# Kernel tuning notes

Measured on AMD Instinct MI355X. Metric: run time of the kernel, lower is better.

The kernel has to match this reference:

```python
import jax, jax.numpy as jnp
import numpy as np

B, E, N, F = 8, 2048, 2048, 128

def setup_inputs() -> dict:
    key = jax.random.key(0)
    k1, k2, k3, k4 = jax.random.split(key, 4)
    node_embeddings = jax.random.normal(k1, (B, N, F), dtype=jnp.float32)
    adj = jax.random.randint(k2, (B, E, N), -1, 3).astype(jnp.float32)
    W = jax.random.normal(k3, (F, F), dtype=jnp.float32) * (1.0 / np.sqrt(F))
    b = jax.random.normal(k4, (F,), dtype=jnp.float32) * 0.01
    return {"node_embeddings": node_embeddings, "adj": adj, "W": W, "b": b}

def reference(node_embeddings, adj, W, b):
    # adj_target: 1 where adj == -1, else 0
    adj_target = (adj == -1).astype(node_embeddings.dtype)          # [B, E, N]
    norm = jnp.sum(adj_target, axis=-1, keepdims=True)               # [B, E, 1]
    norm = jnp.where(norm == 0, 1.0, norm)
    # masked-mean aggregation of neighbor vertices into hyperedges
    message_vertex = jnp.matmul(adj_target, node_embeddings) / norm  # [B, E, F]
    # linear (torch Linear: x @ W.T + b) + relu
    hyperedge_embeddings = jax.nn.relu(jnp.matmul(message_vertex, W.T) + b)
    return hyperedge_embeddings
```

## Files before the change

### kernel.cpp

```cpp
#include <hip/hip_runtime.h>
#include <hip/hip_bf16.h>

#define B_ 8
#define E_ 2048
#define N_ 2048
#define F_ 128

#define BM 16
#define BK 64
#define MP 136

using bf16x8 = __bf16 __attribute__((ext_vector_type(8)));
using fx4    = float __attribute__((ext_vector_type(4)));

__global__ __launch_bounds__(256) void prep_node(const float* __restrict__ node,
                                                 __bf16* __restrict__ nodeT) {
    const int bid = blockIdx.x;
    const int b   = bid & 7;
    const int n0  = (bid >> 3) * 32;
    const int t   = threadIdx.x;
    const int f   = t & 127;
    const int nb  = n0 + (t >> 7) * 16;

    const float* src = node + ((size_t)b * N_ + nb) * F_ + f;
    __bf16 h[16];
#pragma unroll
    for (int i = 0; i < 16; ++i)
        h[i] = (__bf16)src[(size_t)i * F_];

    __bf16* dst = nodeT + ((size_t)b * F_ + f) * N_ + nb;
    *(uint4*)&dst[0] = *(const uint4*)&h[0];
    *(uint4*)&dst[8] = *(const uint4*)&h[8];
}

__global__ __launch_bounds__(256) void prep_w(const float* __restrict__ W,
                                              __bf16* __restrict__ Wb) {
    int idx = blockIdx.x * 256 + threadIdx.x;
    float4 v = *(const float4*)&W[idx * 4];
    __bf16 o[4] = {(__bf16)v.x, (__bf16)v.y, (__bf16)v.z, (__bf16)v.w};
    *(uint2*)&Wb[idx * 4] = *(const uint2*)o;
}

__global__ __launch_bounds__(256) void prep_adj(const float* __restrict__ adj,
                                                unsigned char* __restrict__ bitsT,
                                                float* __restrict__ rcount) {
    __shared__ __align__(16) unsigned char rowB[256];
    __shared__ float cw[4];
    const int row = blockIdx.x;
    const int t   = threadIdx.x;

    const float* src = adj + (size_t)row * N_ + t * 8;
    float4 v0 = *(const float4*)src;
    float4 v1 = *(const float4*)(src + 4);
    unsigned m = 0;
    m |= (v0.x == -1.f) ? 1u   : 0u;
    m |= (v0.y == -1.f) ? 2u   : 0u;
    m |= (v0.z == -1.f) ? 4u   : 0u;
    m |= (v0.w == -1.f) ? 8u   : 0u;
    m |= (v1.x == -1.f) ? 16u  : 0u;
    m |= (v1.y == -1.f) ? 32u  : 0u;
    m |= (v1.z == -1.f) ? 64u  : 0u;
    m |= (v1.w == -1.f) ? 128u : 0u;

    const int q  = t & 3;
    const int ks = (t >> 2) & 1;
    const int mm = t >> 3;
    rowB[q * 64 + mm * 2 + ks] = (unsigned char)m;

    float c = (float)__popc(m);
#pragma unroll
    for (int s = 1; s < 64; s <<= 1) c += __shfl_xor(c, s);
    if ((t & 63) == 0) cw[t >> 6] = c;
    __syncthreads();

    if (t < 64) {
        unsigned d = *(const unsigned*)&rowB[t * 4];
        *(unsigned*)&bitsT[(size_t)row * 256 + t * 4] = d;
    }
    if (t == 0) {
        float tot = cw[0] + cw[1] + cw[2] + cw[3];
        rcount[row] = 1.f / fmaxf(tot, 1.f);
    }
}

__global__ __launch_bounds__(256, 4) void v2h_main(const unsigned char* __restrict__ bitsT,
                                                   const __bf16* __restrict__ nodeT,
                                                   const __bf16* __restrict__ Wb,
                                                   const float* __restrict__ bias,
                                                   const float* __restrict__ rcount,
                                                   float* __restrict__ out) {
    __shared__ __align__(16) __bf16 Bs[2][128][64];
    __shared__ __align__(16) __bf16 Ms[BM * MP];

    const int t    = threadIdx.x;
    const int bid  = blockIdx.x;
    const int b    = bid & 7;
    const int e0   = (bid >> 3) * BM;
    const int w    = t >> 6;
    const int lane = t & 63;
    const int l15  = lane & 15;
    const int quad = lane >> 4;

    const __bf16* nTB = nodeT + (size_t)b * F_ * N_;

    auto issue_dma = [&](int k0, int buf) {
#pragma unroll
        for (int p = 0; p < 4; ++p) {
            int idx = t + 256 * p;
            int f   = idx >> 3;
            int sl  = idx & 7;
            int g   = sl ^ (f & 7);
            const __bf16* src = nTB + (size_t)f * N_ + k0 + g * 8;
            __bf16* dst = &Bs[buf][0][0] + (size_t)(w * 64 + 256 * p) * 8;
            __builtin_amdgcn_global_load_lds(
                (const __attribute__((address_space(1))) void*)src,
                (__attribute__((address_space(3))) void*)dst, 16, 0, 0);
        }
    };

    const unsigned char* rbP = bitsT + ((size_t)b * E_ + e0 + l15) * 256 + quad * 64;
    uint4 rb0 = *(const uint4*)(rbP +  0);
    uint4 rb1 = *(const uint4*)(rbP + 16);
    uint4 rb2 = *(const uint4*)(rbP + 32);
    uint4 rb3 = *(const uint4*)(rbP + 48);
    unsigned rw[16] = {rb0.x, rb0.y, rb0.z, rb0.w, rb1.x, rb1.y, rb1.z, rb1.w,
                       rb2.x, rb2.y, rb2.z, rb2.w, rb3.x, rb3.y, rb3.z, rb3.w};

    auto unpack = [](unsigned byte) -> bf16x8 {
        union { unsigned u[4]; bf16x8 v; } r;
        r.u[0] = ((byte &   1u) ? 0x3F80u : 0u) | ((byte &   2u) ? 0x3F800000u : 0u);
        r.u[1] = ((byte &   4u) ? 0x3F80u : 0u) | ((byte &   8u) ? 0x3F800000u : 0u);
        r.u[2] = ((byte &  16u) ? 0x3F80u : 0u) | ((byte &  32u) ? 0x3F800000u : 0u);
        r.u[3] = ((byte &  64u) ? 0x3F80u : 0u) | ((byte & 128u) ? 0x3F800000u : 0u);
        return r.v;
    };

    fx4 acc[2] = {};

    issue_dma(0, 0);

#pragma unroll
    for (int m = 0; m < 32; ++m) {
        const int buf = m & 1;
        __syncthreads();

        issue_dma(((m + 1) & 31) * BK, buf ^ 1);

        const unsigned word = rw[m >> 1];
        const int sh = 16 * (m & 1);
        bf16x8 af0 = unpack((word >> sh) & 255u);
        bf16x8 af1 = unpack((word >> (sh + 8)) & 255u);

#pragma unroll
        for (int ft = 0; ft < 2; ++ft) {
            int f  = w * 32 + ft * 16 + l15;
            int q0 = quad ^ (f & 7);
            int q1 = (4 + quad) ^ (f & 7);
            bf16x8 b0 = *(const bf16x8*)&Bs[buf][f][q0 * 8];
            acc[ft] = __builtin_amdgcn_mfma_f32_16x16x32_bf16(af0, b0, acc[ft], 0, 0, 0);
            bf16x8 b1 = *(const bf16x8*)&Bs[buf][f][q1 * 8];
            acc[ft] = __builtin_amdgcn_mfma_f32_16x16x32_bf16(af1, b1, acc[ft], 0, 0, 0);
        }
    }

    const int rbase = quad * 4;
    float rn[4];
#pragma unroll
    for (int r = 0; r < 4; ++r)
        rn[r] = rcount[(size_t)b * E_ + e0 + rbase + r];
#pragma unroll
    for (int ft = 0; ft < 2; ++ft) {
        int fcol = w * 32 + ft * 16 + l15;
#pragma unroll
        for (int r = 0; r < 4; ++r)
            Ms[(rbase + r) * MP + fcol] = (__bf16)(acc[ft][r] * rn[r]);
    }
    __syncthreads();

    fx4 acc2[2] = {};
#pragma unroll
    for (int ks = 0; ks < 4; ++ks) {
        bf16x8 afm = *(const bf16x8*)&Ms[l15 * MP + ks * 32 + quad * 8];
#pragma unroll
        for (int gt = 0; gt < 2; ++gt) {
            int g = w * 32 + gt * 16 + l15;
            bf16x8 wfr = *(const bf16x8*)&Wb[(size_t)g * F_ + ks * 32 + quad * 8];
            acc2[gt] = __builtin_amdgcn_mfma_f32_16x16x32_bf16(afm, wfr, acc2[gt], 0, 0, 0);
        }
    }

#pragma unroll
    for (int gt = 0; gt < 2; ++gt) {
        int g = w * 32 + gt * 16 + l15;
        float bb = bias[g];
#pragma unroll
        for (int r = 0; r < 4; ++r) {
            int e = e0 + rbase + r;
            float v = acc2[gt][r] + bb;
            out[((size_t)b * E_ + e) * F_ + g] = fmaxf(v, 0.f);
        }
    }
}

extern "C" void kernel_launch(void* const* d_in, const int* in_sizes, int n_in,
                              void* d_out, int out_size, void* d_ws, size_t ws_size,
                              hipStream_t stream) {
    const float* node = (const float*)d_in[0];
    const float* adj  = (const float*)d_in[1];
    const float* W    = (const float*)d_in[2];
    const float* bias = (const float*)d_in[3];
    float* out = (float*)d_out;

    char* ws = (char*)d_ws;
    __bf16*        nodeT = (__bf16*)ws;
    __bf16*        Wb    = (__bf16*)(ws + 8 * 1024 * 1024);
    unsigned char* bitsT = (unsigned char*)(ws + 8 * 1024 * 1024 + 65536);
    float*         rcnt  = (float*)(ws + 12 * 1024 * 1024 + 65536);

    prep_node<<<512, 256, 0, stream>>>(node, nodeT);
    prep_w<<<16, 256, 0, stream>>>(W, Wb);
    prep_adj<<<B_ * E_, 256, 0, stream>>>(adj, bitsT, rcnt);
    v2h_main<<<1024, 256, 0, stream>>>(bitsT, nodeT, Wb, bias, rcnt, out);
}
```

Measured before the change: 230.6 us.

## Merge prep kernels into one launch and double hyperedge rows per block

Combines the three preprocessing kernels (node transpose, weight cast, adjacency bitmask) into one kernel that branches on block index, which saves two launches. The main kernel now handles 32 hyperedge rows per block instead of 16, so each staged node tile in LDS feeds twice as many MFMAs and total node-tile traffic is halved. The cost is more registers per thread (launch bounds lowered to 2 waves per SIMD) and half as many blocks (512), which may reduce occupancy and latency hiding.

```diff
diff --git a/kernel.cpp b/kernel.cpp
--- a/kernel.cpp
+++ b/kernel.cpp
@@ -6,84 +6,81 @@
 #define N_ 2048
 #define F_ 128
 
-#define BM 16
+#define BM 32
 #define BK 64
 #define MP 136
 
 using bf16x8 = __bf16 __attribute__((ext_vector_type(8)));
 using fx4    = float __attribute__((ext_vector_type(4)));
 
-__global__ __launch_bounds__(256) void prep_node(const float* __restrict__ node,
-                                                 __bf16* __restrict__ nodeT) {
-    const int bid = blockIdx.x;
-    const int b   = bid & 7;
-    const int n0  = (bid >> 3) * 32;
-    const int t   = threadIdx.x;
-    const int f   = t & 127;
-    const int nb  = n0 + (t >> 7) * 16;
-
-    const float* src = node + ((size_t)b * N_ + nb) * F_ + f;
-    __bf16 h[16];
-#pragma unroll
-    for (int i = 0; i < 16; ++i)
-        h[i] = (__bf16)src[(size_t)i * F_];
-
-    __bf16* dst = nodeT + ((size_t)b * F_ + f) * N_ + nb;
-    *(uint4*)&dst[0] = *(const uint4*)&h[0];
-    *(uint4*)&dst[8] = *(const uint4*)&h[8];
-}
-
-__global__ __launch_bounds__(256) void prep_w(const float* __restrict__ W,
-                                              __bf16* __restrict__ Wb) {
-    int idx = blockIdx.x * 256 + threadIdx.x;
-    float4 v = *(const float4*)&W[idx * 4];
-    __bf16 o[4] = {(__bf16)v.x, (__bf16)v.y, (__bf16)v.z, (__bf16)v.w};
-    *(uint2*)&Wb[idx * 4] = *(const uint2*)o;
-}
-
-__global__ __launch_bounds__(256) void prep_adj(const float* __restrict__ adj,
+__global__ __launch_bounds__(256) void prep_all(const float* __restrict__ node,
+                                                const float* __restrict__ adj,
+                                                const float* __restrict__ W,
+                                                __bf16* __restrict__ nodeT,
+                                                __bf16* __restrict__ Wb,
                                                 unsigned char* __restrict__ bitsT,
                                                 float* __restrict__ rcount) {
     __shared__ __align__(16) unsigned char rowB[256];
     __shared__ float cw[4];
-    const int row = blockIdx.x;
+    const int bid = blockIdx.x;
     const int t   = threadIdx.x;
 
-    const float* src = adj + (size_t)row * N_ + t * 8;
-    float4 v0 = *(const float4*)src;
-    float4 v1 = *(const float4*)(src + 4);
-    unsigned m = 0;
-    m |= (v0.x == -1.f) ? 1u   : 0u;
-    m |= (v0.y == -1.f) ? 2u   : 0u;
-    m |= (v0.z == -1.f) ? 4u   : 0u;
-    m |= (v0.w == -1.f) ? 8u   : 0u;
-    m |= (v1.x == -1.f) ? 16u  : 0u;
-    m |= (v1.y == -1.f) ? 32u  : 0u;
-    m |= (v1.z == -1.f) ? 64u  : 0u;
-    m |= (v1.w == -1.f) ? 128u : 0u;
-
-    const int q  = t & 3;
-    const int ks = (t >> 2) & 1;
-    const int mm = t >> 3;
-    rowB[q * 64 + mm * 2 + ks] = (unsigned char)m;
-
-    float c = (float)__popc(m);
-#pragma unroll
-    for (int s = 1; s < 64; s <<= 1) c += __shfl_xor(c, s);
-    if ((t & 63) == 0) cw[t >> 6] = c;
-    __syncthreads();
-
-    if (t < 64) {
-        unsigned d = *(const unsigned*)&rowB[t * 4];
-        *(unsigned*)&bitsT[(size_t)row * 256 + t * 4] = d;
-    }
-    if (t == 0) {
-        float tot = cw[0] + cw[1] + cw[2] + cw[3];
-        rcount[row] = 1.f / fmaxf(tot, 1.f);
+    if (bid < 512) {
+        const int b  = bid & 7;
+        const int n0 = (bid >> 3) * 32;
+        const int f  = t & 127;
+        const int nb = n0 + (t >> 7) * 16;
+        const float* src = node + ((size_t)b * N_ + nb) * F_ + f;
+        __bf16 h[16];
+#pragma unroll
+        for (int i = 0; i < 16; ++i)
+            h[i] = (__bf16)src[(size_t)i * F_];
+        __bf16* dst = nodeT + ((size_t)b * F_ + f) * N_ + nb;
+        *(uint4*)&dst[0] = *(const uint4*)&h[0];
+        *(uint4*)&dst[8] = *(const uint4*)&h[8];
+    } else if (bid < 528) {
+        int idx = (bid - 512) * 256 + t;
+        float4 v = *(const float4*)&W[idx * 4];
+        __bf16 o[4] = {(__bf16)v.x, (__bf16)v.y, (__bf16)v.z, (__bf16)v.w};
+        *(uint2*)&Wb[idx * 4] = *(const uint2*)o;
+    } else {
+        const int row = bid - 528;
+        const float* src = adj + (size_t)row * N_ + t * 8;
+        float4 v0 = *(const float4*)src;
+        float4 v1 = *(const float4*)(src + 4);
+        unsigned m = 0;
+        m |= (v0.x == -1.f) ? 1u   : 0u;
+        m |= (v0.y == -1.f) ? 2u   : 0u;
+        m |= (v0.z == -1.f) ? 4u   : 0u;
+        m |= (v0.w == -1.f) ? 8u   : 0u;
+        m |= (v1.x == -1.f) ? 16u  : 0u;
+        m |= (v1.y == -1.f) ? 32u  : 0u;
+        m |= (v1.z == -1.f) ? 64u  : 0u;
+        m |= (v1.w == -1.f) ? 128u : 0u;
+
+        const int q  = t & 3;
+        const int ks = (t >> 2) & 1;
+        const int mm = t >> 3;
+        rowB[q * 64 + mm * 2 + ks] = (unsigned char)m;
+
+        float c = (float)__popc(m);
+#pragma unroll
+        for (int s = 1; s < 64; s <<= 1) c += __shfl_xor(c, s);
+        if ((t & 63) == 0) cw[t >> 6] = c;
+        __syncthreads();
+
+        if (t < 64) {
+            unsigned d = *(const unsigned*)&rowB[t * 4];
+            *(unsigned*)&bitsT[(size_t)row * 256 + t * 4] = d;
+        }
+        if (t == 0) {
+            float tot = cw[0] + cw[1] + cw[2] + cw[3];
+            rcount[row] = 1.f / fmaxf(tot, 1.f);
+        }
     }
 }
 
-__global__ __launch_bounds__(256, 4) void v2h_main(const unsigned char* __restrict__ bitsT,
+__global__ __launch_bounds__(256, 2) void v2h_main(const unsigned char* __restrict__ bitsT,
                                                    const __bf16* __restrict__ nodeT,
                                                    const __bf16* __restrict__ Wb,
                                                    const float* __restrict__ bias,
@@ -118,13 +115,16 @@
         }
     };
 
-    const unsigned char* rbP = bitsT + ((size_t)b * E_ + e0 + l15) * 256 + quad * 64;
-    uint4 rb0 = *(const uint4*)(rbP +  0);
-    uint4 rb1 = *(const uint4*)(rbP + 16);
-    uint4 rb2 = *(const uint4*)(rbP + 32);
-    uint4 rb3 = *(const uint4*)(rbP + 48);
-    unsigned rw[16] = {rb0.x, rb0.y, rb0.z, rb0.w, rb1.x, rb1.y, rb1.z, rb1.w,
-                       rb2.x, rb2.y, rb2.z, rb2.w, rb3.x, rb3.y, rb3.z, rb3.w};
+    const unsigned char* rpA = bitsT + ((size_t)b * E_ + e0 + l15) * 256 + quad * 64;
+    const unsigned char* rpB = rpA + 16 * 256;
+    uint4 ra0 = *(const uint4*)(rpA +  0), ra1 = *(const uint4*)(rpA + 16);
+    uint4 ra2 = *(const uint4*)(rpA + 32), ra3 = *(const uint4*)(rpA + 48);
+    uint4 rb0 = *(const uint4*)(rpB +  0), rb1 = *(const uint4*)(rpB + 16);
+    uint4 rb2 = *(const uint4*)(rpB + 32), rb3 = *(const uint4*)(rpB + 48);
+    unsigned rwA[16] = {ra0.x, ra0.y, ra0.z, ra0.w, ra1.x, ra1.y, ra1.z, ra1.w,
+                        ra2.x, ra2.y, ra2.z, ra2.w, ra3.x, ra3.y, ra3.z, ra3.w};
+    unsigned rwB[16] = {rb0.x, rb0.y, rb0.z, rb0.w, rb1.x, rb1.y, rb1.z, rb1.w,
+                        rb2.x, rb2.y, rb2.z, rb2.w, rb3.x, rb3.y, rb3.z, rb3.w};
 
     auto unpack = [](unsigned byte) -> bf16x8 {
         union { unsigned u[4]; bf16x8 v; } r;
@@ -135,7 +135,8 @@
         return r.v;
     };
 
-    fx4 acc[2] = {};
+    fx4 accA[2] = {};
+    fx4 accB[2] = {};
 
     issue_dma(0, 0);
 
@@ -146,10 +147,13 @@
 
         issue_dma(((m + 1) & 31) * BK, buf ^ 1);
 
-        const unsigned word = rw[m >> 1];
         const int sh = 16 * (m & 1);
-        bf16x8 af0 = unpack((word >> sh) & 255u);
-        bf16x8 af1 = unpack((word >> (sh + 8)) & 255u);
+        const unsigned wA = rwA[m >> 1] >> sh;
+        const unsigned wB = rwB[m >> 1] >> sh;
+        bf16x8 afA0 = unpack(wA & 255u);
+        bf16x8 afA1 = unpack((wA >> 8) & 255u);
+        bf16x8 afB0 = unpack(wB & 255u);
+        bf16x8 afB1 = unpack((wB >> 8) & 255u);
 
 #pragma unroll
         for (int ft = 0; ft < 2; ++ft) {
@@ -157,35 +161,44 @@
             int q0 = quad ^ (f & 7);
             int q1 = (4 + quad) ^ (f & 7);
             bf16x8 b0 = *(const bf16x8*)&Bs[buf][f][q0 * 8];
-            acc[ft] = __builtin_amdgcn_mfma_f32_16x16x32_bf16(af0, b0, acc[ft], 0, 0, 0);
+            accA[ft] = __builtin_amdgcn_mfma_f32_16x16x32_bf16(afA0, b0, accA[ft], 0, 0, 0);
+            accB[ft] = __builtin_amdgcn_mfma_f32_16x16x32_bf16(afB0, b0, accB[ft], 0, 0, 0);
             bf16x8 b1 = *(const bf16x8*)&Bs[buf][f][q1 * 8];
-            acc[ft] = __builtin_amdgcn_mfma_f32_16x16x32_bf16(af1, b1, acc[ft], 0, 0, 0);
+            accA[ft] = __builtin_amdgcn_mfma_f32_16x16x32_bf16(afA1, b1, accA[ft], 0, 0, 0);
+            accB[ft] = __builtin_amdgcn_mfma_f32_16x16x32_bf16(afB1, b1, accB[ft], 0, 0, 0);
         }
     }
 
     const int rbase = quad * 4;
-    float rn[4];
-#pragma unroll
-    for (int r = 0; r < 4; ++r)
-        rn[r] = rcount[(size_t)b * E_ + e0 + rbase + r];
+    const float* rcB = rcount + (size_t)b * E_ + e0;
+    float rnA[4], rnB[4];
+#pragma unroll
+    for (int r = 0; r < 4; ++r) {
+        rnA[r] = rcB[rbase + r];
+        rnB[r] = rcB[16 + rbase + r];
+    }
 #pragma unroll
     for (int ft = 0; ft < 2; ++ft) {
         int fcol = w * 32 + ft * 16 + l15;
 #pragma unroll
-        for (int r = 0; r < 4; ++r)
-            Ms[(rbase + r) * MP + fcol] = (__bf16)(acc[ft][r] * rn[r]);
+        for (int r = 0; r < 4; ++r) {
+            Ms[(rbase + r) * MP + fcol]      = (__bf16)(accA[ft][r] * rnA[r]);
+            Ms[(16 + rbase + r) * MP + fcol] = (__bf16)(accB[ft][r] * rnB[r]);
+        }
     }
     __syncthreads();
 
-    fx4 acc2[2] = {};
+    fx4 acc2A[2] = {}, acc2B[2] = {};
 #pragma unroll
     for (int ks = 0; ks < 4; ++ks) {
-        bf16x8 afm = *(const bf16x8*)&Ms[l15 * MP + ks * 32 + quad * 8];
+        bf16x8 afmA = *(const bf16x8*)&Ms[l15 * MP + ks * 32 + quad * 8];
+        bf16x8 afmB = *(const bf16x8*)&Ms[(16 + l15) * MP + ks * 32 + quad * 8];
 #pragma unroll
         for (int gt = 0; gt < 2; ++gt) {
             int g = w * 32 + gt * 16 + l15;
             bf16x8 wfr = *(const bf16x8*)&Wb[(size_t)g * F_ + ks * 32 + quad * 8];
-            acc2[gt] = __builtin_amdgcn_mfma_f32_16x16x32_bf16(afm, wfr, acc2[gt], 0, 0, 0);
+            acc2A[gt] = __builtin_amdgcn_mfma_f32_16x16x32_bf16(afmA, wfr, acc2A[gt], 0, 0, 0);
+            acc2B[gt] = __builtin_amdgcn_mfma_f32_16x16x32_bf16(afmB, wfr, acc2B[gt], 0, 0, 0);
         }
     }
 
@@ -196,8 +209,10 @@
 #pragma unroll
         for (int r = 0; r < 4; ++r) {
             int e = e0 + rbase + r;
-            float v = acc2[gt][r] + bb;
-            out[((size_t)b * E_ + e) * F_ + g] = fmaxf(v, 0.f);
+            float vA = acc2A[gt][r] + bb;
+            float vB = acc2B[gt][r] + bb;
+            out[((size_t)b * E_ + e) * F_ + g]      = fmaxf(vA, 0.f);
+            out[((size_t)b * E_ + e + 16) * F_ + g] = fmaxf(vB, 0.f);
         }
     }
 }
@@ -217,8 +232,6 @@
     unsigned char* bitsT = (unsigned char*)(ws + 8 * 1024 * 1024 + 65536);
     float*         rcnt  = (float*)(ws + 12 * 1024 * 1024 + 65536);
 
-    prep_node<<<512, 256, 0, stream>>>(node, nodeT);
-    prep_w<<<16, 256, 0, stream>>>(W, Wb);
-    prep_adj<<<B_ * E_, 256, 0, stream>>>(adj, bitsT, rcnt);
-    v2h_main<<<1024, 256, 0, stream>>>(bitsT, nodeT, Wb, bias, rcnt, out);
+    prep_all<<<528 + B_ * E_, 256, 0, stream>>>(node, adj, W, nodeT, Wb, bitsT, rcnt);
+    v2h_main<<<512, 256, 0, stream>>>(bitsT, nodeT, Wb, bias, rcnt, out);
 }
```

Result: faster. 221.5 us (-4.0%).
